# Performance work log

Measured on AMD Instinct MI355X. Metric: run time of the kernel, lower is better.

The kernel has to match this reference:

```python
import jax, jax.numpy as jnp
import numpy as np

B, N, D, H = 256, 1000, 256, 8
DH = D // H
NEG = -1e9
TANH_CLIP = 10.0


def setup_inputs() -> dict:
    key = jax.random.key(0)
    ks = jax.random.split(key, 16)
    f = jax.random.normal
    return {
        "node_embeddings": f(ks[0], (B, N, D), jnp.float32),
        "graph_context": f(ks[1], (B, D), jnp.float32),
        "glimpse_key": f(ks[2], (B, H, N, DH), jnp.float32),
        "glimpse_val": f(ks[3], (B, H, N, DH), jnp.float32),
        "logit_key": f(ks[4], (B, N, D), jnp.float32),
        "capacity": jax.random.uniform(ks[5], (B, 1, 1), jnp.float32),
        "remaining_demand": jax.random.uniform(ks[6], (B, 1, 1), jnp.float32),
        "remaining_nodes": jax.random.uniform(ks[7], (B, 1, 1), jnp.float32),
        "W_ctx": f(ks[8], (2 * D + 3, 2 * D), jnp.float32) / np.sqrt(2 * D + 3),
        "W_out": f(ks[9], (D, D), jnp.float32) / np.sqrt(D),
        "W_sa": f(ks[10], (D, D), jnp.float32) / np.sqrt(D),
        "head": jax.random.randint(ks[11], (B,), 0, N),
        "feasible_nodes": jax.random.randint(ks[12], (B, N), 0, 2, dtype=jnp.int32),
    }


def _mha(q, k, v, mask):
    # q: [B,H,1,DH]; k,v: [B,H,N,DH]; mask: [B,N] True = feasible
    scores = jnp.einsum('bhqd,bhnd->bhqn', q, k) / np.sqrt(DH)
    scores = jnp.where(mask[:, None, None, :], scores, NEG)
    attn = jax.nn.softmax(scores, axis=-1)
    out = jnp.einsum('bhqn,bhnd->bhqd', attn, v)  # [B,H,1,DH]
    return out.transpose(0, 2, 1, 3).reshape(out.shape[0], D)  # [B,D]


def reference(node_embeddings, graph_context, glimpse_key, glimpse_val,
              logit_key, capacity, remaining_demand, remaining_nodes,
              W_ctx, W_out, W_sa, head, feasible_nodes):
    mask = feasible_nodes.astype(bool)
    no_feasible = ~jnp.any(mask, axis=-1)
    mask = mask.at[:, 0].set(mask[:, 0] | no_feasible)  # force node 0 feasible if all masked

    # dynamic features: [B,3]
    dyn = jnp.concatenate([capacity[:, 0], remaining_demand[:, 0], remaining_nodes[:, 0]], axis=-1)
    # current head node embedding via gather_by_index: [B,D]
    cur = jnp.take_along_axis(node_embeddings, head[:, None, None], axis=1)[:, 0]
    step_context = jnp.concatenate([cur, graph_context, dyn], axis=-1) @ W_ctx  # [B,2D]
    glimpse_q, head_in = step_context[:, :D], step_context[:, D:]

    # glimpse multi-head attention (q_len = 1)
    qh = glimpse_q.reshape(B, 1, H, DH).transpose(0, 2, 1, 3)
    glimpse = _mha(qh, glimpse_key, glimpse_val, mask) @ W_out  # [B,D]

    # single-head pointer logits + tanh clip + masking + log-softmax
    logits = jnp.einsum('bd,bnd->bn', glimpse, logit_key) / np.sqrt(D)
    logits = TANH_CLIP * jnp.tanh(logits)
    logits = jnp.where(mask, logits, NEG)
    log_p = jax.nn.log_softmax(logits, axis=-1)  # [B,N]

    # SimpleSetAttention head encoding over the same cached K/V
    qh2 = head_in.reshape(B, 1, H, DH).transpose(0, 2, 1, 3)
    head_encoding = _mha(qh2, glimpse_key, glimpse_val, mask) @ W_sa  # [B,D]
    return log_p, head_encoding
```

## Files before the change

### kernel.cpp

```cpp
#include <hip/hip_runtime.h>
#include <math.h>

#define B 256
#define N 1000
#define D 256
#define H 8
#define DH 32
#define NEG (-1000000000.0f)

__device__ __forceinline__ float waveReduceMax(float v) {
#pragma unroll
    for (int off = 32; off >= 1; off >>= 1) v = fmaxf(v, __shfl_xor(v, off, 64));
    return v;
}
__device__ __forceinline__ float waveReduceSum(float v) {
#pragma unroll
    for (int off = 32; off >= 1; off >>= 1) v += __shfl_xor(v, off, 64);
    return v;
}

__device__ __forceinline__ float qxor1_add(float v) {
    int t = __builtin_amdgcn_update_dpp(0, __float_as_int(v), 0xB1, 0xF, 0xF, true);
    return v + __int_as_float(t);
}
__device__ __forceinline__ float qxor2_add(float v) {
    int t = __builtin_amdgcn_update_dpp(0, __float_as_int(v), 0x4E, 0xF, 0xF, true);
    return v + __int_as_float(t);
}
__device__ __forceinline__ float sxor4_add(float v) {
    int t = __builtin_amdgcn_ds_swizzle(__float_as_int(v), 0x101F);
    return v + __int_as_float(t);
}
__device__ __forceinline__ float dot4(float4 a, float4 b) {
    return a.x * b.x + a.y * b.y + a.z * b.z + a.w * b.w;
}

__global__ __launch_bounds__(256) void k_mask(
    const int* __restrict__ feas, int* __restrict__ mask_ws)
{
    __shared__ int sRed[4];
    const int b = blockIdx.x;
    const int tid = threadIdx.x;
    int vals[4];
    int orloc = 0;
#pragma unroll
    for (int k = 0; k < 4; ++k) {
        int n = tid + k * 256;
        int v = (n < N) ? feas[b * N + n] : 0;
        vals[k] = v;
        orloc |= v;
    }
#pragma unroll
    for (int off = 32; off >= 1; off >>= 1) orloc |= __shfl_xor(orloc, off, 64);
    if ((tid & 63) == 0) sRed[tid >> 6] = orloc;
    __syncthreads();
    const int anyf = sRed[0] | sRed[1] | sRed[2] | sRed[3];
#pragma unroll
    for (int k = 0; k < 4; ++k) {
        int n = tid + k * 256;
        if (n < N) {
            int m = vals[k];
            if (n == 0 && !anyf) m = 1;
            mask_ws[b * N + n] = m;
        }
    }
}

__global__ __launch_bounds__(256) void k_ctx(
    const float* __restrict__ ne, const float* __restrict__ gc,
    const float* __restrict__ cap, const float* __restrict__ dem,
    const float* __restrict__ rem, const float* __restrict__ Wctx,
    const int* __restrict__ head,
    float* __restrict__ q1_ws, float* __restrict__ q2_ws)
{
    __shared__ float xs[515];
    const int tid = threadIdx.x;
    const int b = blockIdx.x >> 1;
    const int half = blockIdx.x & 1;
    const int hd = head[b];
    for (int i = tid; i < 515; i += 256) {
        float v;
        if (i < 256)       v = ne[(size_t)(b * N + hd) * D + i];
        else if (i < 512)  v = gc[b * D + (i - 256)];
        else if (i == 512) v = cap[b];
        else if (i == 513) v = dem[b];
        else               v = rem[b];
        xs[i] = v;
    }
    __syncthreads();
    const float* __restrict__ wcol = Wctx + half * 256 + tid;
    float a0 = 0.f, a1 = 0.f, a2 = 0.f, a3 = 0.f;
    int i = 0;
#pragma unroll 2
    for (; i + 4 <= 515; i += 4) {
        a0 = fmaf(xs[i + 0], wcol[(i + 0) * 512], a0);
        a1 = fmaf(xs[i + 1], wcol[(i + 1) * 512], a1);
        a2 = fmaf(xs[i + 2], wcol[(i + 2) * 512], a2);
        a3 = fmaf(xs[i + 3], wcol[(i + 3) * 512], a3);
    }
    for (; i < 515; ++i) a0 = fmaf(xs[i], wcol[i * 512], a0);
    float a = (a0 + a1) + (a2 + a3);
    (half ? q2_ws : q1_ws)[b * D + tid] = a;
}

__global__ __launch_bounds__(256) void k_attn(
    const float* __restrict__ gk, const float* __restrict__ gv,
    const float* __restrict__ q1_ws, const float* __restrict__ q2_ws,
    const int* __restrict__ mask_ws,
    float* __restrict__ out1_ws, float* __restrict__ out2_ws)
{
    __shared__ float s1[N];
    __shared__ float s2[N];
    __shared__ float redA[4], redB[4];
    __shared__ __align__(16) float part1[4][DH];
    __shared__ __align__(16) float part2[4][DH];

    const int tid = threadIdx.x;
    const int b = blockIdx.x >> 3;
    const int h = blockIdx.x & 7;
    const int wid = tid >> 6;
    const int lane = tid & 63;
    const int nsub = lane >> 3;
    const int d4 = lane & 7;

    const float4 q1v = ((const float4*)(q1_ws + (size_t)b * D + h * DH))[d4];
    const float4 q2v = ((const float4*)(q2_ws + (size_t)b * D + h * DH))[d4];
    const float scale = 0.17677669529663687f;
    const float4* __restrict__ kb = (const float4*)(gk + (size_t)(b * H + h) * N * DH);
    const int rb8 = wid * 64 + nsub;

#pragma unroll 1
    for (int base = 0; base < 768; base += 256) {
        float4 kv[8];
#pragma unroll
        for (int k = 0; k < 8; ++k) kv[k] = kb[(base + rb8 + k * 8) * 8 + d4];
#pragma unroll
        for (int k = 0; k < 8; ++k) {
            float d1 = dot4(kv[k], q1v);
            float d2 = dot4(kv[k], q2v);
            d1 = qxor1_add(d1); d1 = qxor2_add(d1); d1 = sxor4_add(d1);
            d2 = qxor1_add(d2); d2 = qxor2_add(d2); d2 = sxor4_add(d2);
            if (d4 == 0) {
                int r = base + rb8 + k * 8;
                s1[r] = d1 * scale;
                s2[r] = d2 * scale;
            }
        }
    }
    {
        float4 kv[8];
        int rr[8];
#pragma unroll
        for (int k = 0; k < 8; ++k) {
            rr[k] = 768 + rb8 + k * 8;
            kv[k] = (rr[k] < N) ? kb[rr[k] * 8 + d4] : make_float4(0.f, 0.f, 0.f, 0.f);
        }
#pragma unroll
        for (int k = 0; k < 8; ++k) {
            float d1 = dot4(kv[k], q1v);
            float d2 = dot4(kv[k], q2v);
            d1 = qxor1_add(d1); d1 = qxor2_add(d1); d1 = sxor4_add(d1);
            d2 = qxor1_add(d2); d2 = qxor2_add(d2); d2 = sxor4_add(d2);
            if (d4 == 0 && rr[k] < N) {
                s1[rr[k]] = d1 * scale;
                s2[rr[k]] = d2 * scale;
            }
        }
    }
    __syncthreads();

    float m1 = -INFINITY, m2 = -INFINITY;
    float v1[4], v2[4];
#pragma unroll
    for (int k = 0; k < 4; ++k) {
        int n = tid + k * 256;
        if (n < N) {
            int mm = mask_ws[b * N + n];
            v1[k] = mm ? s1[n] : NEG;
            v2[k] = mm ? s2[n] : NEG;
            m1 = fmaxf(m1, v1[k]);
            m2 = fmaxf(m2, v2[k]);
        } else { v1[k] = NEG; v2[k] = NEG; }
    }
    m1 = waveReduceMax(m1);
    m2 = waveReduceMax(m2);
    if ((tid & 63) == 0) { redA[wid] = m1; redB[wid] = m2; }
    __syncthreads();
    m1 = fmaxf(fmaxf(redA[0], redA[1]), fmaxf(redA[2], redA[3]));
    m2 = fmaxf(fmaxf(redB[0], redB[1]), fmaxf(redB[2], redB[3]));
    __syncthreads();

    float sum1 = 0.f, sum2 = 0.f;
#pragma unroll
    for (int k = 0; k < 4; ++k) {
        int n = tid + k * 256;
        if (n < N) {
            float e1 = __expf(v1[k] - m1);
            float e2 = __expf(v2[k] - m2);
            s1[n] = e1; s2[n] = e2;
            sum1 += e1; sum2 += e2;
        }
    }
    sum1 = waveReduceSum(sum1);
    sum2 = waveReduceSum(sum2);
    if ((tid & 63) == 0) { redA[wid] = sum1; redB[wid] = sum2; }
    __syncthreads();
    sum1 = redA[0] + redA[1] + redA[2] + redA[3];
    sum2 = redB[0] + redB[1] + redB[2] + redB[3];

    const float4* __restrict__ vb = (const float4*)(gv + (size_t)(b * H + h) * N * DH);
    float4 a1 = {0.f, 0.f, 0.f, 0.f}, a2 = {0.f, 0.f, 0.f, 0.f};
#pragma unroll 1
    for (int base = 0; base < 768; base += 256) {
        float4 vv[8];
#pragma unroll
        for (int k = 0; k < 8; ++k) vv[k] = vb[(base + rb8 + k * 8) * 8 + d4];
#pragma unroll
        for (int k = 0; k < 8; ++k) {
            int r = base + rb8 + k * 8;
            float p1 = s1[r], p2 = s2[r];
            a1.x = fmaf(p1, vv[k].x, a1.x); a1.y = fmaf(p1, vv[k].y, a1.y);
            a1.z = fmaf(p1, vv[k].z, a1.z); a1.w = fmaf(p1, vv[k].w, a1.w);
            a2.x = fmaf(p2, vv[k].x, a2.x); a2.y = fmaf(p2, vv[k].y, a2.y);
            a2.z = fmaf(p2, vv[k].z, a2.z); a2.w = fmaf(p2, vv[k].w, a2.w);
        }
    }
    {
        float4 vv[8];
        int rr[8];
#pragma unroll
        for (int k = 0; k < 8; ++k) {
            rr[k] = 768 + rb8 + k * 8;
            vv[k] = (rr[k] < N) ? vb[rr[k] * 8 + d4] : make_float4(0.f, 0.f, 0.f, 0.f);
        }
#pragma unroll
        for (int k = 0; k < 8; ++k) {
            float p1 = (rr[k] < N) ? s1[rr[k]] : 0.f;
            float p2 = (rr[k] < N) ? s2[rr[k]] : 0.f;
            a1.x = fmaf(p1, vv[k].x, a1.x); a1.y = fmaf(p1, vv[k].y, a1.y);
            a1.z = fmaf(p1, vv[k].z, a1.z); a1.w = fmaf(p1, vv[k].w, a1.w);
            a2.x = fmaf(p2, vv[k].x, a2.x); a2.y = fmaf(p2, vv[k].y, a2.y);
            a2.z = fmaf(p2, vv[k].z, a2.z); a2.w = fmaf(p2, vv[k].w, a2.w);
        }
    }
#pragma unroll
    for (int off = 8; off <= 32; off <<= 1) {
        a1.x += __shfl_xor(a1.x, off, 64); a1.y += __shfl_xor(a1.y, off, 64);
        a1.z += __shfl_xor(a1.z, off, 64); a1.w += __shfl_xor(a1.w, off, 64);
        a2.x += __shfl_xor(a2.x, off, 64); a2.y += __shfl_xor(a2.y, off, 64);
        a2.z += __shfl_xor(a2.z, off, 64); a2.w += __shfl_xor(a2.w, off, 64);
    }
    if (lane < 8) {
        ((float4*)part1[wid])[d4] = a1;
        ((float4*)part2[wid])[d4] = a2;
    }
    __syncthreads();

    if (tid < 64) {
        int set = tid >> 5, d = tid & 31;
        float tot = set ? (part2[0][d] + part2[1][d] + part2[2][d] + part2[3][d])
                        : (part1[0][d] + part1[1][d] + part1[2][d] + part1[3][d]);
        float rs = 1.f / (set ? sum2 : sum1);
        (set ? out2_ws : out1_ws)[b * D + h * DH + d] = tot * rs;
    }
}

__global__ __launch_bounds__(256) void k_proj(
    const float* __restrict__ out1_ws, const float* __restrict__ out2_ws,
    const float* __restrict__ Wout, const float* __restrict__ Wsa,
    float* __restrict__ glimpse_ws, float* __restrict__ head_enc)
{
    __shared__ float x[D];
    const int tid = threadIdx.x;
    const int b = blockIdx.x >> 1;
    const int which = blockIdx.x & 1;
    const float* __restrict__ src = which ? out2_ws : out1_ws;
    x[tid] = src[b * D + tid];
    __syncthreads();
    const float* __restrict__ W = which ? Wsa : Wout;
    float a = 0.f;
#pragma unroll 8
    for (int i = 0; i < D; ++i) a = fmaf(x[i], W[i * D + tid], a);
    (which ? head_enc : glimpse_ws)[b * D + tid] = a;
}

__global__ __launch_bounds__(256) void k_logits(
    const float* __restrict__ lk, const float* __restrict__ glimpse_ws,
    const int* __restrict__ mask_ws, float* __restrict__ logits_ws)
{
    __shared__ __align__(16) float gsh[D];
    const int tid = threadIdx.x;
    const int b = blockIdx.x >> 2;
    const int chunk = blockIdx.x & 3;
    gsh[tid] = glimpse_ws[b * D + tid];
    __syncthreads();

    const int lane = tid & 63, wid = tid >> 6;
    const int rs = lane >> 3;
    const int c  = lane & 7;
    float4 g[8];
#pragma unroll
    for (int j = 0; j < 8; ++j) g[j] = ((const float4*)gsh)[c + 8 * j];

    const int n0 = chunk * 250;
    const int nend = n0 + 250;
    const float4* __restrict__ lkb = (const float4*)(lk + (size_t)b * N * D);

#pragma unroll 1
    for (int it = 0; it < 8; ++it) {
        const int r = n0 + it * 32 + wid * 8 + rs;
        const bool ok = (r < nend);
        float4 kv[8];
#pragma unroll
        for (int j = 0; j < 8; ++j)
            kv[j] = ok ? lkb[(size_t)r * 64 + c + 8 * j]
                       : make_float4(0.f, 0.f, 0.f, 0.f);
        float p = 0.f;
#pragma unroll
        for (int j = 0; j < 8; ++j) p += dot4(kv[j], g[j]);
        p = qxor1_add(p); p = qxor2_add(p); p = sxor4_add(p);
        if (c == 0 && ok) {
            float l = 10.0f * tanhf(p * 0.0625f);
            logits_ws[b * N + r] = mask_ws[b * N + r] ? l : NEG;
        }
    }
}

__global__ __launch_bounds__(256) void k_logsoftmax(
    const float* __restrict__ logits_ws, float* __restrict__ logp)
{
    __shared__ float red[4];
    const int tid = threadIdx.x;
    const int b = blockIdx.x;
    float v[4];
    float m = -INFINITY;
#pragma unroll
    for (int k = 0; k < 4; ++k) {
        int n = tid + k * 256;
        v[k] = (n < N) ? logits_ws[b * N + n] : -INFINITY;
        m = fmaxf(m, v[k]);
    }
    m = waveReduceMax(m);
    if ((tid & 63) == 0) red[tid >> 6] = m;
    __syncthreads();
    m = fmaxf(fmaxf(red[0], red[1]), fmaxf(red[2], red[3]));
    __syncthreads();
    float s = 0.f;
#pragma unroll
    for (int k = 0; k < 4; ++k) {
        int n = tid + k * 256;
        if (n < N) s += __expf(v[k] - m);
    }
    s = waveReduceSum(s);
    if ((tid & 63) == 0) red[tid >> 6] = s;
    __syncthreads();
    s = red[0] + red[1] + red[2] + red[3];
    const float lse = m + logf(s);
#pragma unroll
    for (int k = 0; k < 4; ++k) {
        int n = tid + k * 256;
        if (n < N) logp[b * N + n] = v[k] - lse;
    }
}

extern "C" void kernel_launch(void* const* d_in, const int* in_sizes, int n_in,
                              void* d_out, int out_size, void* d_ws, size_t ws_size,
                              hipStream_t stream) {
    const float* ne   = (const float*)d_in[0];
    const float* gc   = (const float*)d_in[1];
    const float* gk   = (const float*)d_in[2];
    const float* gvv  = (const float*)d_in[3];
    const float* lk   = (const float*)d_in[4];
    const float* cap  = (const float*)d_in[5];
    const float* dem  = (const float*)d_in[6];
    const float* rem  = (const float*)d_in[7];
    const float* Wctx = (const float*)d_in[8];
    const float* Wout = (const float*)d_in[9];
    const float* Wsa  = (const float*)d_in[10];
    const int*   head = (const int*)d_in[11];
    const int*   feas = (const int*)d_in[12];
    float* out = (float*)d_out;

    float* ws        = (float*)d_ws;
    float* q1_ws     = ws;
    float* q2_ws     = q1_ws + B * D;
    int*   mask_ws   = (int*)(q2_ws + B * D);
    float* out1_ws   = (float*)(mask_ws + B * N);
    float* out2_ws   = out1_ws + B * D;
    float* glimpse_ws= out2_ws + B * D;
    float* logits_ws = glimpse_ws + B * D;

    hipLaunchKernelGGL(k_mask, dim3(B), dim3(256), 0, stream, feas, mask_ws);
    hipLaunchKernelGGL(k_ctx, dim3(B * 2), dim3(256), 0, stream,
                       ne, gc, cap, dem, rem, Wctx, head, q1_ws, q2_ws);
    hipLaunchKernelGGL(k_attn, dim3(B * H), dim3(256), 0, stream,
                       gk, gvv, q1_ws, q2_ws, mask_ws, out1_ws, out2_ws);
    hipLaunchKernelGGL(k_proj, dim3(B * 2), dim3(256), 0, stream,
                       out1_ws, out2_ws, Wout, Wsa, glimpse_ws, out + B * N);
    hipLaunchKernelGGL(k_logits, dim3(B * 4), dim3(256), 0, stream,
                       lk, glimpse_ws, mask_ws, logits_ws);
    hipLaunchKernelGGL(k_logsoftmax, dim3(B), dim3(256), 0, stream,
                       logits_ws, out);
}
```

Baseline: 815.0 us.

## Fuse mask, attention, projection, logits and log-softmax into one per-batch kernel

Replaces five kernels (mask, attn, proj, logits, logsoftmax) with a single 1024-thread block per batch row that keeps the mask, scores, attention outputs, glimpse and logits in shared memory. This removes launch overhead and the workspace round trips through global memory between stages. In exchange, the grid shrinks from 2048 blocks of 256 threads to 256 blocks of 1024 threads, and the kernel uses a large shared-memory footprint (about 70KB). That can cut occupancy and parallelism on a GPU with many CUs. The logits stage now streams the logit_key rows from a single block per batch instead of four.

New measurement: 791.5 us, median of 2. 1.03x faster.

```diff
diff --git a/kernel.cpp b/kernel.cpp
--- a/kernel.cpp
+++ b/kernel.cpp
@@ -18,7 +18,6 @@
     for (int off = 32; off >= 1; off >>= 1) v += __shfl_xor(v, off, 64);
     return v;
 }
-
 __device__ __forceinline__ float qxor1_add(float v) {
     int t = __builtin_amdgcn_update_dpp(0, __float_as_int(v), 0xB1, 0xF, 0xF, true);
     return v + __int_as_float(t);
@@ -33,37 +32,6 @@
 }
 __device__ __forceinline__ float dot4(float4 a, float4 b) {
     return a.x * b.x + a.y * b.y + a.z * b.z + a.w * b.w;
-}
-
-__global__ __launch_bounds__(256) void k_mask(
-    const int* __restrict__ feas, int* __restrict__ mask_ws)
-{
-    __shared__ int sRed[4];
-    const int b = blockIdx.x;
-    const int tid = threadIdx.x;
-    int vals[4];
-    int orloc = 0;
-#pragma unroll
-    for (int k = 0; k < 4; ++k) {
-        int n = tid + k * 256;
-        int v = (n < N) ? feas[b * N + n] : 0;
-        vals[k] = v;
-        orloc |= v;
-    }
-#pragma unroll
-    for (int off = 32; off >= 1; off >>= 1) orloc |= __shfl_xor(orloc, off, 64);
-    if ((tid & 63) == 0) sRed[tid >> 6] = orloc;
-    __syncthreads();
-    const int anyf = sRed[0] | sRed[1] | sRed[2] | sRed[3];
-#pragma unroll
-    for (int k = 0; k < 4; ++k) {
-        int n = tid + k * 256;
-        if (n < N) {
-            int m = vals[k];
-            if (n == 0 && !anyf) m = 1;
-            mask_ws[b * N + n] = m;
-        }
-    }
 }
 
 __global__ __launch_bounds__(256) void k_ctx(
@@ -103,37 +71,68 @@
     (half ? q2_ws : q1_ws)[b * D + tid] = a;
 }
 
-__global__ __launch_bounds__(256) void k_attn(
+__global__ __launch_bounds__(1024) void k_mega(
     const float* __restrict__ gk, const float* __restrict__ gv,
+    const float* __restrict__ lk,
     const float* __restrict__ q1_ws, const float* __restrict__ q2_ws,
-    const int* __restrict__ mask_ws,
-    float* __restrict__ out1_ws, float* __restrict__ out2_ws)
+    const float* __restrict__ Wout, const float* __restrict__ Wsa,
+    const int* __restrict__ feas,
+    float* __restrict__ logp, float* __restrict__ henc_out)
 {
-    __shared__ float s1[N];
-    __shared__ float s2[N];
-    __shared__ float redA[4], redB[4];
-    __shared__ __align__(16) float part1[4][DH];
-    __shared__ __align__(16) float part2[4][DH];
-
-    const int tid = threadIdx.x;
-    const int b = blockIdx.x >> 3;
-    const int h = blockIdx.x & 7;
-    const int wid = tid >> 6;
+    __shared__ float s1[H][N];
+    __shared__ float s2[H][N];
+    __shared__ int   smask[N];
+    __shared__ __align__(16) float q1s[D];
+    __shared__ __align__(16) float q2s[D];
+    __shared__ int   redOi[16];
+    __shared__ float redSum[H][2];
+    __shared__ __align__(16) float part1[H][2][DH];
+    __shared__ __align__(16) float part2[H][2][DH];
+    __shared__ float out1s[D], out2s[D];
+    __shared__ float gpart[2][D], hpart[2][D];
+    __shared__ __align__(16) float glimpse_s[D];
+    __shared__ float logits_s[N];
+    __shared__ float redM[16], redS[16];
+
+    const int tid  = threadIdx.x;
+    const int b    = blockIdx.x;
+    const int wid  = tid >> 6;
     const int lane = tid & 63;
+
+    int mv = (tid < N) ? feas[b * N + tid] : 0;
+    int orloc = mv;
+#pragma unroll
+    for (int off = 32; off >= 1; off >>= 1) orloc |= __shfl_xor(orloc, off, 64);
+    if (lane == 0) redOi[wid] = orloc;
+    if (tid < 512) {
+        float qv = (tid < 256 ? q1_ws : q2_ws)[b * D + (tid & 255)];
+        (tid < 256 ? q1s : q2s)[tid & 255] = qv;
+    }
+    __syncthreads();
+    if (tid < N) {
+        int anyf = 0;
+#pragma unroll
+        for (int i = 0; i < 16; ++i) anyf |= redOi[i];
+        smask[tid] = (tid == 0 && !anyf) ? 1 : mv;
+    }
+    __syncthreads();
+
+    const int h    = wid >> 1;
+    const int half = wid & 1;
     const int nsub = lane >> 3;
-    const int d4 = lane & 7;
-
-    const float4 q1v = ((const float4*)(q1_ws + (size_t)b * D + h * DH))[d4];
-    const float4 q2v = ((const float4*)(q2_ws + (size_t)b * D + h * DH))[d4];
+    const int d4   = lane & 7;
+    const int r0   = half * 8 + nsub;
+    const float4 q1v = ((const float4*)(q1s + h * DH))[d4];
+    const float4 q2v = ((const float4*)(q2s + h * DH))[d4];
     const float scale = 0.17677669529663687f;
     const float4* __restrict__ kb = (const float4*)(gk + (size_t)(b * H + h) * N * DH);
-    const int rb8 = wid * 64 + nsub;
 
 #pragma unroll 1
-    for (int base = 0; base < 768; base += 256) {
+    for (int it = 0; it < 7; ++it) {
+        const int rbase = it * 128 + r0;
         float4 kv[8];
 #pragma unroll
-        for (int k = 0; k < 8; ++k) kv[k] = kb[(base + rb8 + k * 8) * 8 + d4];
+        for (int k = 0; k < 8; ++k) kv[k] = kb[(rbase + 16 * k) * 8 + d4];
 #pragma unroll
         for (int k = 0; k < 8; ++k) {
             float d1 = dot4(kv[k], q1v);
@@ -141,18 +140,18 @@
             d1 = qxor1_add(d1); d1 = qxor2_add(d1); d1 = sxor4_add(d1);
             d2 = qxor1_add(d2); d2 = qxor2_add(d2); d2 = sxor4_add(d2);
             if (d4 == 0) {
-                int r = base + rb8 + k * 8;
-                s1[r] = d1 * scale;
-                s2[r] = d2 * scale;
+                int r = rbase + 16 * k;
+                int m = smask[r];
+                s1[h][r] = m ? d1 * scale : NEG;
+                s2[h][r] = m ? d2 * scale : NEG;
             }
         }
     }
     {
-        float4 kv[8];
-        int rr[8];
-#pragma unroll
-        for (int k = 0; k < 8; ++k) {
-            rr[k] = 768 + rb8 + k * 8;
+        float4 kv[8]; int rr[8];
+#pragma unroll
+        for (int k = 0; k < 8; ++k) {
+            rr[k] = 896 + r0 + 16 * k;
             kv[k] = (rr[k] < N) ? kb[rr[k] * 8 + d4] : make_float4(0.f, 0.f, 0.f, 0.f);
         }
 #pragma unroll
@@ -162,63 +161,46 @@
             d1 = qxor1_add(d1); d1 = qxor2_add(d1); d1 = sxor4_add(d1);
             d2 = qxor1_add(d2); d2 = qxor2_add(d2); d2 = sxor4_add(d2);
             if (d4 == 0 && rr[k] < N) {
-                s1[rr[k]] = d1 * scale;
-                s2[rr[k]] = d2 * scale;
+                int m = smask[rr[k]];
+                s1[h][rr[k]] = m ? d1 * scale : NEG;
+                s2[h][rr[k]] = m ? d2 * scale : NEG;
             }
         }
     }
     __syncthreads();
 
-    float m1 = -INFINITY, m2 = -INFINITY;
-    float v1[4], v2[4];
-#pragma unroll
-    for (int k = 0; k < 4; ++k) {
-        int n = tid + k * 256;
-        if (n < N) {
-            int mm = mask_ws[b * N + n];
-            v1[k] = mm ? s1[n] : NEG;
-            v2[k] = mm ? s2[n] : NEG;
-            m1 = fmaxf(m1, v1[k]);
-            m2 = fmaxf(m2, v2[k]);
-        } else { v1[k] = NEG; v2[k] = NEG; }
-    }
-    m1 = waveReduceMax(m1);
-    m2 = waveReduceMax(m2);
-    if ((tid & 63) == 0) { redA[wid] = m1; redB[wid] = m2; }
-    __syncthreads();
-    m1 = fmaxf(fmaxf(redA[0], redA[1]), fmaxf(redA[2], redA[3]));
-    m2 = fmaxf(fmaxf(redB[0], redB[1]), fmaxf(redB[2], redB[3]));
-    __syncthreads();
-
-    float sum1 = 0.f, sum2 = 0.f;
-#pragma unroll
-    for (int k = 0; k < 4; ++k) {
-        int n = tid + k * 256;
-        if (n < N) {
-            float e1 = __expf(v1[k] - m1);
-            float e2 = __expf(v2[k] - m2);
-            s1[n] = e1; s2[n] = e2;
-            sum1 += e1; sum2 += e2;
-        }
-    }
-    sum1 = waveReduceSum(sum1);
-    sum2 = waveReduceSum(sum2);
-    if ((tid & 63) == 0) { redA[wid] = sum1; redB[wid] = sum2; }
-    __syncthreads();
-    sum1 = redA[0] + redA[1] + redA[2] + redA[3];
-    sum2 = redB[0] + redB[1] + redB[2] + redB[3];
+    {
+        float* __restrict__ sarr = (wid & 1) ? s2[wid >> 1] : s1[wid >> 1];
+        float mx = -INFINITY;
+#pragma unroll
+        for (int t = 0; t < 16; ++t) {
+            int r = lane + 64 * t;
+            if (r < N) mx = fmaxf(mx, sarr[r]);
+        }
+        mx = waveReduceMax(mx);
+        float sum = 0.f;
+#pragma unroll
+        for (int t = 0; t < 16; ++t) {
+            int r = lane + 64 * t;
+            if (r < N) { float e = __expf(sarr[r] - mx); sarr[r] = e; sum += e; }
+        }
+        sum = waveReduceSum(sum);
+        if (lane == 0) redSum[wid >> 1][wid & 1] = sum;
+    }
+    __syncthreads();
 
     const float4* __restrict__ vb = (const float4*)(gv + (size_t)(b * H + h) * N * DH);
     float4 a1 = {0.f, 0.f, 0.f, 0.f}, a2 = {0.f, 0.f, 0.f, 0.f};
 #pragma unroll 1
-    for (int base = 0; base < 768; base += 256) {
+    for (int it = 0; it < 7; ++it) {
+        const int rbase = it * 128 + r0;
         float4 vv[8];
 #pragma unroll
-        for (int k = 0; k < 8; ++k) vv[k] = vb[(base + rb8 + k * 8) * 8 + d4];
-#pragma unroll
-        for (int k = 0; k < 8; ++k) {
-            int r = base + rb8 + k * 8;
-            float p1 = s1[r], p2 = s2[r];
+        for (int k = 0; k < 8; ++k) vv[k] = vb[(rbase + 16 * k) * 8 + d4];
+#pragma unroll
+        for (int k = 0; k < 8; ++k) {
+            int r = rbase + 16 * k;
+            float p1 = s1[h][r], p2 = s2[h][r];
             a1.x = fmaf(p1, vv[k].x, a1.x); a1.y = fmaf(p1, vv[k].y, a1.y);
             a1.z = fmaf(p1, vv[k].z, a1.z); a1.w = fmaf(p1, vv[k].w, a1.w);
             a2.x = fmaf(p2, vv[k].x, a2.x); a2.y = fmaf(p2, vv[k].y, a2.y);
@@ -226,17 +208,16 @@
         }
     }
     {
-        float4 vv[8];
-        int rr[8];
-#pragma unroll
-        for (int k = 0; k < 8; ++k) {
-            rr[k] = 768 + rb8 + k * 8;
+        float4 vv[8]; int rr[8];
+#pragma unroll
+        for (int k = 0; k < 8; ++k) {
+            rr[k] = 896 + r0 + 16 * k;
             vv[k] = (rr[k] < N) ? vb[rr[k] * 8 + d4] : make_float4(0.f, 0.f, 0.f, 0.f);
         }
 #pragma unroll
         for (int k = 0; k < 8; ++k) {
-            float p1 = (rr[k] < N) ? s1[rr[k]] : 0.f;
-            float p2 = (rr[k] < N) ? s2[rr[k]] : 0.f;
+            float p1 = (rr[k] < N) ? s1[h][rr[k]] : 0.f;
+            float p2 = (rr[k] < N) ? s2[h][rr[k]] : 0.f;
             a1.x = fmaf(p1, vv[k].x, a1.x); a1.y = fmaf(p1, vv[k].y, a1.y);
             a1.z = fmaf(p1, vv[k].z, a1.z); a1.w = fmaf(p1, vv[k].w, a1.w);
             a2.x = fmaf(p2, vv[k].x, a2.x); a2.y = fmaf(p2, vv[k].y, a2.y);
@@ -251,115 +232,94 @@
         a2.z += __shfl_xor(a2.z, off, 64); a2.w += __shfl_xor(a2.w, off, 64);
     }
     if (lane < 8) {
-        ((float4*)part1[wid])[d4] = a1;
-        ((float4*)part2[wid])[d4] = a2;
-    }
-    __syncthreads();
-
-    if (tid < 64) {
-        int set = tid >> 5, d = tid & 31;
-        float tot = set ? (part2[0][d] + part2[1][d] + part2[2][d] + part2[3][d])
-                        : (part1[0][d] + part1[1][d] + part1[2][d] + part1[3][d]);
-        float rs = 1.f / (set ? sum2 : sum1);
-        (set ? out2_ws : out1_ws)[b * D + h * DH + d] = tot * rs;
-    }
-}
-
-__global__ __launch_bounds__(256) void k_proj(
-    const float* __restrict__ out1_ws, const float* __restrict__ out2_ws,
-    const float* __restrict__ Wout, const float* __restrict__ Wsa,
-    float* __restrict__ glimpse_ws, float* __restrict__ head_enc)
-{
-    __shared__ float x[D];
-    const int tid = threadIdx.x;
-    const int b = blockIdx.x >> 1;
-    const int which = blockIdx.x & 1;
-    const float* __restrict__ src = which ? out2_ws : out1_ws;
-    x[tid] = src[b * D + tid];
-    __syncthreads();
-    const float* __restrict__ W = which ? Wsa : Wout;
-    float a = 0.f;
-#pragma unroll 8
-    for (int i = 0; i < D; ++i) a = fmaf(x[i], W[i * D + tid], a);
-    (which ? head_enc : glimpse_ws)[b * D + tid] = a;
-}
-
-__global__ __launch_bounds__(256) void k_logits(
-    const float* __restrict__ lk, const float* __restrict__ glimpse_ws,
-    const int* __restrict__ mask_ws, float* __restrict__ logits_ws)
-{
-    __shared__ __align__(16) float gsh[D];
-    const int tid = threadIdx.x;
-    const int b = blockIdx.x >> 2;
-    const int chunk = blockIdx.x & 3;
-    gsh[tid] = glimpse_ws[b * D + tid];
-    __syncthreads();
-
-    const int lane = tid & 63, wid = tid >> 6;
-    const int rs = lane >> 3;
-    const int c  = lane & 7;
-    float4 g[8];
-#pragma unroll
-    for (int j = 0; j < 8; ++j) g[j] = ((const float4*)gsh)[c + 8 * j];
-
-    const int n0 = chunk * 250;
-    const int nend = n0 + 250;
-    const float4* __restrict__ lkb = (const float4*)(lk + (size_t)b * N * D);
-
+        ((float4*)part1[h][half])[d4] = a1;
+        ((float4*)part2[h][half])[d4] = a2;
+    }
+    __syncthreads();
+    if (tid < 512) {
+        int hh = (tid & 255) >> 5, d = tid & 31;
+        if (tid < 256) {
+            float rs = 1.f / redSum[hh][0];
+            out1s[tid] = (part1[hh][0][d] + part1[hh][1][d]) * rs;
+        } else {
+            float rs = 1.f / redSum[hh][1];
+            out2s[tid - 256] = (part2[hh][0][d] + part2[hh][1][d]) * rs;
+        }
+    }
+    __syncthreads();
+
+    {
+        const int col = tid & 255;
+        const int seg = (tid >> 8) & 1;
+        const bool isG = tid < 512;
+        const float* __restrict__ W  = isG ? Wout : Wsa;
+        const float* __restrict__ xv = isG ? out1s : out2s;
+        const float* __restrict__ Wp = W + (size_t)(seg * 128) * D + col;
+        const float* __restrict__ xp = xv + seg * 128;
+        float c0 = 0.f, c1 = 0.f, c2 = 0.f, c3 = 0.f;
+#pragma unroll 2
+        for (int i = 0; i < 128; i += 4) {
+            c0 = fmaf(xp[i + 0], Wp[(i + 0) * D], c0);
+            c1 = fmaf(xp[i + 1], Wp[(i + 1) * D], c1);
+            c2 = fmaf(xp[i + 2], Wp[(i + 2) * D], c2);
+            c3 = fmaf(xp[i + 3], Wp[(i + 3) * D], c3);
+        }
+        (isG ? gpart : hpart)[seg][col] = (c0 + c1) + (c2 + c3);
+    }
+    __syncthreads();
+    if (tid < 256) {
+        glimpse_s[tid] = gpart[0][tid] + gpart[1][tid];
+    } else if (tid < 512) {
+        int c = tid - 256;
+        henc_out[b * D + c] = hpart[0][c] + hpart[1][c];
+    }
+    __syncthreads();
+
+    {
+        const int rs = lane >> 3;
+        const int c  = lane & 7;
+        float4 g[8];
+#pragma unroll
+        for (int j = 0; j < 8; ++j) g[j] = ((const float4*)glimpse_s)[c + 8 * j];
+        const float4* __restrict__ lkb = (const float4*)(lk + (size_t)b * N * D);
 #pragma unroll 1
-    for (int it = 0; it < 8; ++it) {
-        const int r = n0 + it * 32 + wid * 8 + rs;
-        const bool ok = (r < nend);
-        float4 kv[8];
-#pragma unroll
-        for (int j = 0; j < 8; ++j)
-            kv[j] = ok ? lkb[(size_t)r * 64 + c + 8 * j]
-                       : make_float4(0.f, 0.f, 0.f, 0.f);
-        float p = 0.f;
-#pragma unroll
-        for (int j = 0; j < 8; ++j) p += dot4(kv[j], g[j]);
-        p = qxor1_add(p); p = qxor2_add(p); p = sxor4_add(p);
-        if (c == 0 && ok) {
-            float l = 10.0f * tanhf(p * 0.0625f);
-            logits_ws[b * N + r] = mask_ws[b * N + r] ? l : NEG;
-        }
-    }
-}
-
-__global__ __launch_bounds__(256) void k_logsoftmax(
-    const float* __restrict__ logits_ws, float* __restrict__ logp)
-{
-    __shared__ float red[4];
-    const int tid = threadIdx.x;
-    const int b = blockIdx.x;
-    float v[4];
-    float m = -INFINITY;
-#pragma unroll
-    for (int k = 0; k < 4; ++k) {
-        int n = tid + k * 256;
-        v[k] = (n < N) ? logits_ws[b * N + n] : -INFINITY;
-        m = fmaxf(m, v[k]);
-    }
-    m = waveReduceMax(m);
-    if ((tid & 63) == 0) red[tid >> 6] = m;
-    __syncthreads();
-    m = fmaxf(fmaxf(red[0], red[1]), fmaxf(red[2], red[3]));
-    __syncthreads();
-    float s = 0.f;
-#pragma unroll
-    for (int k = 0; k < 4; ++k) {
-        int n = tid + k * 256;
-        if (n < N) s += __expf(v[k] - m);
-    }
-    s = waveReduceSum(s);
-    if ((tid & 63) == 0) red[tid >> 6] = s;
-    __syncthreads();
-    s = red[0] + red[1] + red[2] + red[3];
-    const float lse = m + logf(s);
-#pragma unroll
-    for (int k = 0; k < 4; ++k) {
-        int n = tid + k * 256;
-        if (n < N) logp[b * N + n] = v[k] - lse;
+        for (int it = 0; it < 8; ++it) {
+            const int r = it * 128 + wid * 8 + rs;
+            const bool ok = (r < N);
+            float4 kv[8];
+#pragma unroll
+            for (int j = 0; j < 8; ++j)
+                kv[j] = ok ? lkb[(size_t)r * 64 + c + 8 * j]
+                           : make_float4(0.f, 0.f, 0.f, 0.f);
+            float p = 0.f;
+#pragma unroll
+            for (int j = 0; j < 8; ++j) p += dot4(kv[j], g[j]);
+            p = qxor1_add(p); p = qxor2_add(p); p = sxor4_add(p);
+            if (c == 0 && ok) {
+                float l = 10.0f * tanhf(p * 0.0625f);
+                logits_s[r] = smask[r] ? l : NEG;
+            }
+        }
+    }
+    __syncthreads();
+
+    {
+        float v = (tid < N) ? logits_s[tid] : -INFINITY;
+        float m = waveReduceMax(v);
+        if (lane == 0) redM[wid] = m;
+        __syncthreads();
+        m = redM[0];
+#pragma unroll
+        for (int i = 1; i < 16; ++i) m = fmaxf(m, redM[i]);
+        float e = (tid < N) ? __expf(v - m) : 0.f;
+        float s = waveReduceSum(e);
+        if (lane == 0) redS[wid] = s;
+        __syncthreads();
+        s = 0.f;
+#pragma unroll
+        for (int i = 0; i < 16; ++i) s += redS[i];
+        const float lse = m + logf(s);
+        if (tid < N) logp[b * N + tid] = v - lse;
     }
 }
 
@@ -381,24 +341,13 @@
     const int*   feas = (const int*)d_in[12];
     float* out = (float*)d_out;
 
-    float* ws        = (float*)d_ws;
-    float* q1_ws     = ws;
-    float* q2_ws     = q1_ws + B * D;
-    int*   mask_ws   = (int*)(q2_ws + B * D);
-    float* out1_ws   = (float*)(mask_ws + B * N);
-    float* out2_ws   = out1_ws + B * D;
-    float* glimpse_ws= out2_ws + B * D;
-    float* logits_ws = glimpse_ws + B * D;
-
-    hipLaunchKernelGGL(k_mask, dim3(B), dim3(256), 0, stream, feas, mask_ws);
+    float* ws    = (float*)d_ws;
+    float* q1_ws = ws;
+    float* q2_ws = q1_ws + B * D;
+
     hipLaunchKernelGGL(k_ctx, dim3(B * 2), dim3(256), 0, stream,
                        ne, gc, cap, dem, rem, Wctx, head, q1_ws, q2_ws);
-    hipLaunchKernelGGL(k_attn, dim3(B * H), dim3(256), 0, stream,
-                       gk, gvv, q1_ws, q2_ws, mask_ws, out1_ws, out2_ws);
-    hipLaunchKernelGGL(k_proj, dim3(B * 2), dim3(256), 0, stream,
-                       out1_ws, out2_ws, Wout, Wsa, glimpse_ws, out + B * N);
-    hipLaunchKernelGGL(k_logits, dim3(B * 4), dim3(256), 0, stream,
-                       lk, glimpse_ws, mask_ws, logits_ws);
-    hipLaunchKernelGGL(k_logsoftmax, dim3(B), dim3(256), 0, stream,
-                       logits_ws, out);
-}
+    hipLaunchKernelGGL(k_mega, dim3(B), dim3(1024), 0, stream,
+                       gk, gvv, lk, q1_ws, q2_ws, Wout, Wsa, feas,
+                       out, out + B * N);
+}
```
